# Kernel optimization log

Hardware: AMD Instinct MI355X
Metric: run time of the kernel (lower is better)

Reference implementation:

```python
import jax, jax.numpy as jnp
import numpy as np

F_FRAMES = 128   # number of frames (seq_start_end rows)
P_PEDS = 32      # pedestrians per frame (uniform)
B = F_FRAMES * P_PEDS
E, H, BN, PM, M = 64, 128, 1024, 512, 1024
PRED_LEN = 12


def setup_inputs() -> dict:
    key = jax.random.key(0)
    ks = jax.random.split(key, 20)
    n = lambda k, s, sc=0.05: (jax.random.normal(k, s) * sc).astype(jnp.float32)
    starts = jnp.arange(F_FRAMES, dtype=jnp.int32) * P_PEDS
    seq_start_end = jnp.stack([starts, starts + P_PEDS], axis=1)
    return {
        "h0": n(ks[0], (1, B, H), 1.0),
        "c0": n(ks[1], (1, B, H), 1.0),
        "obs_final_pos": n(ks[2], (B, 2), 1.0),
        "obs_final_pos_rel": n(ks[3], (B, 2), 1.0),
        "W_emb": n(ks[4], (2, E)), "b_emb": jnp.zeros((E,), jnp.float32),
        "W_ih": n(ks[5], (4 * H, E)), "W_hh": n(ks[6], (4 * H, H)),
        "b_ih": jnp.zeros((4 * H,), jnp.float32), "b_hh": jnp.zeros((4 * H,), jnp.float32),
        "W_pos": n(ks[7], (H, 2)), "b_pos": jnp.zeros((2,), jnp.float32),
        "W_pe": n(ks[8], (2, E)), "b_pe": jnp.zeros((E,), jnp.float32),
        "W_p1": n(ks[9], (E + H, PM)), "b_p1": jnp.zeros((PM,), jnp.float32),
        "W_p2": n(ks[10], (PM, BN)), "b_p2": jnp.zeros((BN,), jnp.float32),
        "W_m1": n(ks[11], (H + BN, M)), "b_m1": jnp.zeros((M,), jnp.float32),
        "W_m2": n(ks[12], (M, H)), "b_m2": jnp.zeros((H,), jnp.float32),
        "seq_start_end": seq_start_end,
    }


def reference(h0, c0, obs_final_pos, obs_final_pos_rel,
              W_emb, b_emb, W_ih, W_hh, b_ih, b_hh, W_pos, b_pos,
              W_pe, b_pe, W_p1, b_p1, W_p2, b_p2, W_m1, b_m1, W_m2, b_m2,
              seq_start_end):
    Bn = h0.shape[1]
    F = seq_start_end.shape[0]
    P = Bn // F  # uniform frame size
    h, c = h0[0], c0[0]
    x0 = obs_final_pos_rel @ W_emb + b_emb  # decoder input embedding

    def step(carry, _):
        x, h, c, last_pos = carry
        # LSTM cell (PyTorch gate order i,f,g,o)
        gates = x @ W_ih.T + h @ W_hh.T + b_ih + b_hh  # (B, 4H)
        i, f, g, o = jnp.split(gates, 4, axis=-1)
        i, f, o = jax.nn.sigmoid(i), jax.nn.sigmoid(f), jax.nn.sigmoid(o)
        c_new = f * c + i * jnp.tanh(g)
        h_new = o * jnp.tanh(c_new)
        rel_pos = h_new @ W_pos + b_pos
        curr_pos = rel_pos + last_pos
        # PoolNet: per-frame pairwise rel-pos embed + MLP + max over neighbours j
        pos = curr_pos.reshape(F, P, 2)
        hf = h_new.reshape(F, P, H)
        rel = pos[:, None, :, :] - pos[:, :, None, :]  # rel[f,i,j] = pos_j - pos_i
        e = rel @ W_pe + b_pe  # (F,P,P,E)
        feat = jnp.concatenate(
            [e, jnp.broadcast_to(hf[:, None], (F, P, P, H))], axis=-1)  # h of j
        z = jax.nn.relu(feat @ W_p1 + b_p1)
        z = jax.nn.relu(z @ W_p2 + b_p2)  # (F,P,P,BN)
        pool_h = z.max(axis=2).reshape(Bn, BN)
        # hidden refresh MLP
        mi = jnp.concatenate([h_new, pool_h], axis=-1)
        nh = jax.nn.relu(mi @ W_m1 + b_m1)
        nh = jax.nn.relu(nh @ W_m2 + b_m2)
        x_new = rel_pos @ W_emb + b_emb
        return (x_new, nh, c_new, curr_pos), (curr_pos, rel_pos)

    _, (pred_seq, pred_seq_rel) = jax.lax.scan(
        jax.checkpoint(step), (x0, h, c, obs_final_pos), None, length=PRED_LEN)
    return pred_seq, pred_seq_rel
```

## Files before the change

kernel.cpp:

```cpp
#include <hip/hip_runtime.h>

#define NB 4096
#define HD 128
#define ED 64
#define NF 128
#define NP 32
#define TSTEPS 12

typedef __attribute__((ext_vector_type(8))) short short8;
typedef __attribute__((ext_vector_type(8))) __bf16 bf16x8;
typedef __attribute__((ext_vector_type(8))) _Float16 f16x8;
typedef __attribute__((ext_vector_type(4))) float f32x4;
typedef __attribute__((ext_vector_type(16))) float f32x16;

#define MFMA16(a, b, c)  __builtin_amdgcn_mfma_f32_16x16x32_bf16((a), (b), (c), 0, 0, 0)
#define MFMA32H(a, b, c) __builtin_amdgcn_mfma_f32_32x32x16_f16((a), (b), (c), 0, 0, 0)

__device__ __forceinline__ unsigned short f2bf(float f) {
  unsigned int x = __float_as_uint(f);
  x += 0x7fffu + ((x >> 16) & 1u);
  return (unsigned short)(x >> 16);
}

__device__ __forceinline__ float sigm(float x) { return 1.0f / (1.0f + expf(-x)); }

__device__ __forceinline__ f16x8 relu8(f16x8 x) {
  return __builtin_elementwise_max(x, (f16x8)(_Float16)0);
}


__global__ __launch_bounds__(256) void k_transpose_bf(const float* __restrict__ W,
                                                      unsigned short* __restrict__ Wt,
                                                      int K, int N) {
  __shared__ float t[32][33];
  int nb = blockIdx.x * 32, kb = blockIdx.y * 32;
  int tx = threadIdx.x & 31, ty = threadIdx.x >> 5;
  #pragma unroll
  for (int r = 0; r < 32; r += 8)
    t[ty + r][tx] = W[(size_t)(kb + ty + r) * N + nb + tx];
  __syncthreads();
  #pragma unroll
  for (int r = 0; r < 32; r += 8)
    Wt[(size_t)(nb + ty + r) * K + kb + tx] = f2bf(t[tx][ty + r]);
}

__global__ __launch_bounds__(256) void k_pack_bfrag32(const float* __restrict__ Wp2,
                                                      _Float16* __restrict__ Bf) {
  int U = blockIdx.x * 256 + threadIdx.x;
  int l = U & 63, cb = (U >> 6) & 31, ks = U >> 11;
  int col = cb * 32 + (l & 31);
  int k0 = ks * 16 + (l >> 5) * 8;
  f16x8 r;
  #pragma unroll
  for (int e = 0; e < 8; ++e) r[e] = (_Float16)Wp2[(size_t)(k0 + e) * 1024 + col];
  *(f16x8*)(Bf + (size_t)U * 8) = r;
}

__global__ __launch_bounds__(256) void k_pack_lstm_w(const float* __restrict__ Wih,
                                                     const float* __restrict__ Whh,
                                                     float* __restrict__ WihT,
                                                     float* __restrict__ WhhT) {
  int idx = blockIdx.x * 256 + threadIdx.x;
  if (idx < 64 * 512) { int k = idx >> 9, n = idx & 511; WihT[idx] = Wih[n * 64 + k]; }
  if (idx < 128 * 512) { int k = idx >> 9, n = idx & 511; WhhT[idx] = Whh[n * 128 + k]; }
}

__global__ __launch_bounds__(256) void k_pack_wpp(const float* __restrict__ Wpe,
                                                  const float* __restrict__ bpe,
                                                  const float* __restrict__ Wp1,
                                                  const float* __restrict__ bp1,
                                                  float* __restrict__ Wpp,
                                                  float* __restrict__ cvec) {
  int n = blockIdx.x * 256 + threadIdx.x;
  if (n >= 512) return;
  float s0 = 0.f, s1 = 0.f, sc = 0.f;
  for (int k = 0; k < 64; ++k) {
    float w = Wp1[k * 512 + n];
    s0 += Wpe[k] * w;
    s1 += Wpe[64 + k] * w;
    sc += bpe[k] * w;
  }
  Wpp[n * 2] = s0; Wpp[n * 2 + 1] = s1; cvec[n] = sc + bp1[n];
}

__global__ __launch_bounds__(256) void k_x0(const float* __restrict__ ofr,
                                            const float* __restrict__ Wemb,
                                            const float* __restrict__ bemb,
                                            float* __restrict__ x) {
  int idx = blockIdx.x * 256 + threadIdx.x;
  if (idx >= NB * ED) return;
  int row = idx >> 6, e = idx & 63;
  x[idx] = bemb[e] + ofr[row * 2] * Wemb[e] + ofr[row * 2 + 1] * Wemb[64 + e];
}


__global__ __launch_bounds__(256) void k12_lstm_uv(
    const float* __restrict__ x, const float* __restrict__ hin, const float* __restrict__ cin,
    const float* __restrict__ WihT, const float* __restrict__ WhhT,
    const float* __restrict__ bih, const float* __restrict__ bhh,
    const float* __restrict__ Wpos, const float* __restrict__ bpos,
    const float* __restrict__ Wemb, const float* __restrict__ bemb,
    const float* __restrict__ lastpos,
    const float* __restrict__ Wp1, const float* __restrict__ Wpp,
    const float* __restrict__ cvec,
    float* __restrict__ cout, unsigned short* __restrict__ mi,
    float* __restrict__ posout, float* __restrict__ xout,
    float* __restrict__ outc, float* __restrict__ outr,
    _Float16* __restrict__ u16, _Float16* __restrict__ v16) {
  __shared__ float xh[8][192];
  __shared__ float hnl[8][128];
  __shared__ float rp[8][2];
  __shared__ float cp[8][2];
  int tid = threadIdx.x;
  int r0 = blockIdx.x * 8;
  for (int idx = tid; idx < 8 * 192; idx += 256) {
    int r = idx / 192, k = idx % 192;
    xh[r][k] = (k < 64) ? x[(r0 + r) * 64 + k] : hin[(r0 + r) * 128 + (k - 64)];
  }
  __syncthreads();
  int j = tid & 127, rg = tid >> 7;
  float acc0[4], acc1[4], acc2[4], acc3[4];
  {
    float b0 = bih[j] + bhh[j];
    float b1 = bih[128 + j] + bhh[128 + j];
    float b2 = bih[256 + j] + bhh[256 + j];
    float b3 = bih[384 + j] + bhh[384 + j];
    #pragma unroll
    for (int r = 0; r < 4; ++r) { acc0[r] = b0; acc1[r] = b1; acc2[r] = b2; acc3[r] = b3; }
  }
  for (int k = 0; k < 64; ++k) {
    float w0 = WihT[k * 512 + j], w1 = WihT[k * 512 + 128 + j],
          w2 = WihT[k * 512 + 256 + j], w3 = WihT[k * 512 + 384 + j];
    #pragma unroll
    for (int r = 0; r < 4; ++r) {
      float xv = xh[rg * 4 + r][k];
      acc0[r] += w0 * xv; acc1[r] += w1 * xv; acc2[r] += w2 * xv; acc3[r] += w3 * xv;
    }
  }
  for (int k = 0; k < 128; ++k) {
    float w0 = WhhT[k * 512 + j], w1 = WhhT[k * 512 + 128 + j],
          w2 = WhhT[k * 512 + 256 + j], w3 = WhhT[k * 512 + 384 + j];
    #pragma unroll
    for (int r = 0; r < 4; ++r) {
      float hv = xh[rg * 4 + r][64 + k];
      acc0[r] += w0 * hv; acc1[r] += w1 * hv; acc2[r] += w2 * hv; acc3[r] += w3 * hv;
    }
  }
  #pragma unroll
  for (int r = 0; r < 4; ++r) {
    int row = r0 + rg * 4 + r;
    float ig = sigm(acc0[r]), fg = sigm(acc1[r]), gg = tanhf(acc2[r]), og = sigm(acc3[r]);
    float cn = fg * cin[row * 128 + j] + ig * gg;
    float hv = og * tanhf(cn);
    cout[row * 128 + j] = cn;
    mi[(size_t)row * 1152 + j] = f2bf(hv);
    hnl[rg * 4 + r][j] = hv;
  }
  __syncthreads();
  {
    int r = tid >> 5;
    int d = (tid >> 4) & 1;
    int l = tid & 15;
    float s = 0.f;
    #pragma unroll
    for (int k = l; k < 128; k += 16) s += hnl[r][k] * Wpos[k * 2 + d];
    s += __shfl_xor(s, 1);
    s += __shfl_xor(s, 2);
    s += __shfl_xor(s, 4);
    s += __shfl_xor(s, 8);
    if (l == 0) {
      int row = r0 + r;
      float rel = s + bpos[d];
      float cur = rel + lastpos[row * 2 + d];
      rp[r][d] = rel;
      cp[r][d] = cur;
      posout[row * 2 + d] = cur;
      outc[row * 2 + d] = cur;
      outr[row * 2 + d] = rel;
    }
  }
  __syncthreads();
  for (int idx = tid; idx < 8 * 64; idx += 256) {
    int r = idx >> 6, e = idx & 63;
    xout[(r0 + r) * 64 + e] = bemb[e] + rp[r][0] * Wemb[e] + rp[r][1] * Wemb[64 + e];
  }
  int n = tid, n2 = tid + 256;
  float aA[8], aB[8];
  #pragma unroll
  for (int r = 0; r < 8; ++r) { aA[r] = 0.f; aB[r] = 0.f; }
  for (int k = 0; k < 128; ++k) {
    float wA = Wp1[(64 + k) * 512 + n], wB = Wp1[(64 + k) * 512 + n2];
    #pragma unroll
    for (int r = 0; r < 8; ++r) { aA[r] += wA * hnl[r][k]; aB[r] += wB * hnl[r][k]; }
  }
  float wp0A = Wpp[n * 2], wp1A = Wpp[n * 2 + 1], cA = cvec[n];
  float wp0B = Wpp[n2 * 2], wp1B = Wpp[n2 * 2 + 1], cB = cvec[n2];
  #pragma unroll
  for (int r = 0; r < 8; ++r) {
    int row = r0 + r;
    float t0 = cp[r][0] * wp0A + cp[r][1] * wp1A;
    v16[(size_t)row * 512 + n] = (_Float16)t0;
    u16[(size_t)row * 512 + n] = (_Float16)(t0 + aA[r] + cA);
    float t1 = cp[r][0] * wp0B + cp[r][1] * wp1B;
    v16[(size_t)row * 512 + n2] = (_Float16)t1;
    u16[(size_t)row * 512 + n2] = (_Float16)(t1 + aB[r] + cB);
  }
}

__global__ __launch_bounds__(256, 2) void k3_pool(
    const _Float16* __restrict__ u16, const _Float16* __restrict__ v16,
    const _Float16* __restrict__ Bf, const float* __restrict__ bp2,
    unsigned short* __restrict__ mi) {
  __shared__ _Float16 u_lds[32 * 512];
  __shared__ _Float16 v_lds[8 * 512];
  int f = blockIdx.x, ig = blockIdx.y, ng = blockIdx.z;
  int tid = threadIdx.x, wid = tid >> 6, lane = tid & 63;
  int r32 = lane & 31, hi = lane >> 5;
  int ip = wid >> 1, nh = wid & 1;

  const f16x8* Bfu = (const f16x8*)Bf;
  int cb0 = ng * 4 + nh * 2;

  f16x8 Bb[8][2];
  #pragma unroll
  for (int s = 0; s < 7; ++s) {
    Bb[s][0] = Bfu[(size_t)((s * 32 + cb0 + 0) * 64 + lane)];
    Bb[s][1] = Bfu[(size_t)((s * 32 + cb0 + 1) * 64 + lane)];
  }

  #pragma unroll
  for (int t = 0; t < 8; ++t) {
    int unit = tid + t * 256;
    int row = unit >> 6, seg = unit & 63;
    f16x8 val = *(const f16x8*)(u16 + (size_t)(f * 32 + row) * 512 + seg * 8);
    int byte = (row << 10) + (seg << 4);
    byte ^= (row & 7) << 4;
    *(f16x8*)((char*)u_lds + byte) = val;
  }
  #pragma unroll
  for (int t = 0; t < 2; ++t) {
    int unit = tid + t * 256;
    int row = unit >> 6, seg = unit & 63;
    *(f16x8*)(v_lds + (row << 9) + seg * 8) =
        *(const f16x8*)(v16 + (size_t)(f * 32 + ig * 8 + row) * 512 + seg * 8);
  }
  __syncthreads();

  f32x16 acc[4][2];
  #pragma unroll
  for (int a = 0; a < 4; ++a)
    #pragma unroll
    for (int n = 0; n < 2; ++n)
      #pragma unroll
      for (int r = 0; r < 16; ++r) acc[a][n][r] = 0.f;

  int ubase = (r32 << 10) + (hi << 4);
  int usw = (r32 & 7) << 4;
  const _Float16* vp = v_lds + ((ip * 4) << 9) + hi * 8;

#define K3STEP(KS)                                                               \
  {                                                                              \
    if ((KS) + 7 < 32) {                                                         \
      Bb[((KS) + 7) & 7][0] = Bfu[(size_t)((((KS) + 7) * 32 + cb0 + 0) * 64 + lane)]; \
      Bb[((KS) + 7) & 7][1] = Bfu[(size_t)((((KS) + 7) * 32 + cb0 + 1) * 64 + lane)]; \
    }                                                                            \
    f16x8 uf = *(const f16x8*)((const char*)u_lds + ((ubase + (KS) * 32) ^ usw));\
    f16x8 a0 = relu8(uf - *(const f16x8*)(vp + (KS) * 16));                      \
    f16x8 a1 = relu8(uf - *(const f16x8*)(vp + 512 + (KS) * 16));                \
    f16x8 a2 = relu8(uf - *(const f16x8*)(vp + 1024 + (KS) * 16));               \
    f16x8 a3 = relu8(uf - *(const f16x8*)(vp + 1536 + (KS) * 16));               \
    __builtin_amdgcn_s_setprio(1);                                               \
    acc[0][0] = MFMA32H(a0, Bb[(KS) & 7][0], acc[0][0]);                         \
    acc[1][0] = MFMA32H(a1, Bb[(KS) & 7][0], acc[1][0]);                         \
    acc[2][0] = MFMA32H(a2, Bb[(KS) & 7][0], acc[2][0]);                         \
    acc[3][0] = MFMA32H(a3, Bb[(KS) & 7][0], acc[3][0]);                         \
    acc[0][1] = MFMA32H(a0, Bb[(KS) & 7][1], acc[0][1]);                         \
    acc[1][1] = MFMA32H(a1, Bb[(KS) & 7][1], acc[1][1]);                         \
    acc[2][1] = MFMA32H(a2, Bb[(KS) & 7][1], acc[2][1]);                         \
    acc[3][1] = MFMA32H(a3, Bb[(KS) & 7][1], acc[3][1]);                         \
    __builtin_amdgcn_s_setprio(0);                                               \
  }

  #pragma unroll
  for (int kk = 0; kk < 32; kk += 8) {
    K3STEP(kk + 0) K3STEP(kk + 1) K3STEP(kk + 2) K3STEP(kk + 3)
    K3STEP(kk + 4) K3STEP(kk + 5) K3STEP(kk + 6) K3STEP(kk + 7)
  }
#undef K3STEP

  #pragma unroll
  for (int ii = 0; ii < 4; ++ii) {
    int rowg = f * 32 + ig * 8 + ip * 4 + ii;
    #pragma unroll
    for (int nt = 0; nt < 2; ++nt) {
      float m = acc[ii][nt][0];
      #pragma unroll
      for (int r = 1; r < 16; ++r) m = fmaxf(m, acc[ii][nt][r]);
      m = fmaxf(m, __shfl_xor(m, 32));
      if (hi == 0) {
        int col = (cb0 + nt) * 32 + r32;
        float val = fmaxf(m + bp2[col], 0.f);
        mi[(size_t)rowg * 1152 + 128 + col] = f2bf(val);
      }
    }
  }
}

__global__ __launch_bounds__(512) void k4_mlp1(
    const unsigned short* __restrict__ mi, const unsigned short* __restrict__ Wt,
    const float* __restrict__ bm1, unsigned short* __restrict__ nh1) {
  int bid = blockIdx.x;
  int mb = bid & 63, nb = bid >> 6;
  int tid = threadIdx.x, wid = tid >> 6, lane = tid & 63;
  int row0 = mb * 64 + (wid >> 2) * 32;
  int nc0 = nb * 256 + (wid & 3) * 64;
  int c = lane & 15, q = lane >> 4;
  const unsigned short* a0p = mi + (size_t)(row0 + c) * 1152;
  const unsigned short* a1p = a0p + 16 * 1152;
  const unsigned short* bb = Wt + (size_t)(nc0 + c) * 1152;
  f32x4 acc[2][4];
  #pragma unroll
  for (int a = 0; a < 2; ++a)
    #pragma unroll
    for (int b = 0; b < 4; ++b) acc[a][b] = (f32x4){0.f, 0.f, 0.f, 0.f};
  for (int ks = 0; ks < 36; ++ks) {
    int k0 = ks * 32 + q * 8;
    bf16x8 a0 = *(const bf16x8*)(a0p + k0);
    bf16x8 a1 = *(const bf16x8*)(a1p + k0);
    #pragma unroll
    for (int nt = 0; nt < 4; ++nt) {
      bf16x8 bf = *(const bf16x8*)(bb + (size_t)nt * 16 * 1152 + k0);
      acc[0][nt] = MFMA16(a0, bf, acc[0][nt]);
      acc[1][nt] = MFMA16(a1, bf, acc[1][nt]);
    }
  }
  #pragma unroll
  for (int mt = 0; mt < 2; ++mt)
    #pragma unroll
    for (int nt = 0; nt < 4; ++nt)
      #pragma unroll
      for (int r = 0; r < 4; ++r) {
        int row = row0 + mt * 16 + q * 4 + r;
        int col = nc0 + nt * 16 + c;
        float val = fmaxf(acc[mt][nt][r] + bm1[col], 0.f);
        nh1[(size_t)row * 1024 + col] = f2bf(val);
      }
}

__global__ __launch_bounds__(128) void k5_mlp2(
    const unsigned short* __restrict__ nh1, const unsigned short* __restrict__ Wt,
    const float* __restrict__ bm2, float* __restrict__ hout) {
  int bid = blockIdx.x;
  int tid = threadIdx.x, wid = tid >> 6, lane = tid & 63;
  int row0 = bid * 16;
  int nc0 = wid * 64;
  int c = lane & 15, q = lane >> 4;
  const unsigned short* ap = nh1 + (size_t)(row0 + c) * 1024;
  const unsigned short* bb = Wt + (size_t)(nc0 + c) * 1024;
  f32x4 acc[4];
  #pragma unroll
  for (int b = 0; b < 4; ++b) acc[b] = (f32x4){0.f, 0.f, 0.f, 0.f};
  for (int ks = 0; ks < 32; ++ks) {
    int k0 = ks * 32 + q * 8;
    bf16x8 a = *(const bf16x8*)(ap + k0);
    #pragma unroll
    for (int nt = 0; nt < 4; ++nt) {
      bf16x8 bf = *(const bf16x8*)(bb + (size_t)nt * 16 * 1024 + k0);
      acc[nt] = MFMA16(a, bf, acc[nt]);
    }
  }
  #pragma unroll
  for (int nt = 0; nt < 4; ++nt)
    #pragma unroll
    for (int r = 0; r < 4; ++r) {
      int row = row0 + q * 4 + r;
      int col = nc0 + nt * 16 + c;
      hout[(size_t)row * 128 + col] = fmaxf(acc[nt][r] + bm2[col], 0.f);
    }
}


extern "C" void kernel_launch(void* const* d_in, const int* in_sizes, int n_in,
                              void* d_out, int out_size, void* d_ws, size_t ws_size,
                              hipStream_t stream) {
  const float* h0   = (const float*)d_in[0];
  const float* c0   = (const float*)d_in[1];
  const float* ofp  = (const float*)d_in[2];
  const float* ofr  = (const float*)d_in[3];
  const float* Wemb = (const float*)d_in[4];
  const float* bemb = (const float*)d_in[5];
  const float* Wih  = (const float*)d_in[6];
  const float* Whh  = (const float*)d_in[7];
  const float* bih  = (const float*)d_in[8];
  const float* bhh  = (const float*)d_in[9];
  const float* Wpos = (const float*)d_in[10];
  const float* bpos = (const float*)d_in[11];
  const float* Wpe  = (const float*)d_in[12];
  const float* bpe  = (const float*)d_in[13];
  const float* Wp1  = (const float*)d_in[14];
  const float* bp1  = (const float*)d_in[15];
  const float* Wp2  = (const float*)d_in[16];
  const float* bp2  = (const float*)d_in[17];
  const float* Wm1  = (const float*)d_in[18];
  const float* bm1  = (const float*)d_in[19];
  const float* Wm2  = (const float*)d_in[20];
  const float* bm2  = (const float*)d_in[21];

  char* ws = (char*)d_ws;
  size_t off = 0;
  auto alloc = [&](size_t bytes) {
    char* p = ws + off;
    off += (bytes + 255) & ~(size_t)255;
    return p;
  };
  float* h    = (float*)alloc((size_t)NB * HD * 4);
  float* cst  = (float*)alloc((size_t)NB * HD * 4);
  float* xbuf = (float*)alloc((size_t)NB * ED * 4);
  float* pos  = (float*)alloc((size_t)NB * 2 * 4);
  _Float16* u16 = (_Float16*)alloc((size_t)NB * 512 * 2);
  _Float16* v16 = (_Float16*)alloc((size_t)NB * 512 * 2);
  unsigned short* mi   = (unsigned short*)alloc((size_t)NB * 1152 * 2);
  unsigned short* nh1  = (unsigned short*)alloc((size_t)NB * 1024 * 2);
  float* WihT = (float*)alloc(64 * 512 * 4);
  float* WhhT = (float*)alloc(128 * 512 * 4);
  float* Wpp  = (float*)alloc(512 * 2 * 4);
  float* cvec = (float*)alloc(512 * 4);
  _Float16* Bf  = (_Float16*)alloc((size_t)1024 * 512 * 2);
  unsigned short* Wm1t = (unsigned short*)alloc((size_t)1024 * 1152 * 2);
  unsigned short* Wm2t = (unsigned short*)alloc((size_t)128 * 1024 * 2);

  float* outc = (float*)d_out;
  float* outr = outc + (size_t)TSTEPS * NB * 2;

  k_pack_lstm_w<<<256, 256, 0, stream>>>(Wih, Whh, WihT, WhhT);
  k_pack_wpp<<<2, 256, 0, stream>>>(Wpe, bpe, Wp1, bp1, Wpp, cvec);
  k_pack_bfrag32<<<256, 256, 0, stream>>>(Wp2, Bf);
  k_transpose_bf<<<dim3(1024 / 32, 1152 / 32), 256, 0, stream>>>(Wm1, Wm1t, 1152, 1024);
  k_transpose_bf<<<dim3(128 / 32, 1024 / 32), 256, 0, stream>>>(Wm2, Wm2t, 1024, 128);
  k_x0<<<NB * ED / 256, 256, 0, stream>>>(ofr, Wemb, bemb, xbuf);

  for (int t = 0; t < TSTEPS; ++t) {
    const float* hin = (t == 0) ? h0 : h;
    const float* cin = (t == 0) ? c0 : cst;
    const float* lp  = (t == 0) ? ofp : pos;
    k12_lstm_uv<<<NB / 8, 256, 0, stream>>>(xbuf, hin, cin, WihT, WhhT, bih, bhh,
                                            Wpos, bpos, Wemb, bemb, lp, Wp1, Wpp, cvec,
                                            cst, mi, pos, xbuf,
                                            outc + (size_t)t * NB * 2,
                                            outr + (size_t)t * NB * 2, u16, v16);
    k3_pool<<<dim3(128, 4, 8), 256, 0, stream>>>(u16, v16, Bf, bp2, mi);
    k4_mlp1<<<256, 512, 0, stream>>>(mi, Wm1t, bm1, nh1);
    k5_mlp2<<<256, 128, 0, stream>>>(nh1, Wm2t, bm2, h);
  }
}
```

Measured before the change: 2.883 ms.

## Split pool kernel work across 8 waves with smaller per-wave accumulator tiles

The pool kernel now runs with 512 threads per block instead of 256. Each wave handles 2 pedestrian rows instead of 4, which halves its accumulator registers, and the B-fragment prefetch depth drops from 7 to 3. The aim is more resident waves per CU to hide LDS and global latency. In exchange, the Wp2 fragments are loaded by twice as many waves, and the shallower prefetch may expose more of the global load latency.

```diff
diff --git a/kernel.cpp b/kernel.cpp
--- a/kernel.cpp
+++ b/kernel.cpp
@@ -207,7 +207,7 @@
   }
 }
 
-__global__ __launch_bounds__(256, 2) void k3_pool(
+__global__ __launch_bounds__(512, 4) void k3_pool(
     const _Float16* __restrict__ u16, const _Float16* __restrict__ v16,
     const _Float16* __restrict__ Bf, const float* __restrict__ bp2,
     unsigned short* __restrict__ mi) {
@@ -221,34 +221,32 @@
   const f16x8* Bfu = (const f16x8*)Bf;
   int cb0 = ng * 4 + nh * 2;
 
-  f16x8 Bb[8][2];
-  #pragma unroll
-  for (int s = 0; s < 7; ++s) {
+  f16x8 Bb[4][2];
+  #pragma unroll
+  for (int s = 0; s < 3; ++s) {
     Bb[s][0] = Bfu[(size_t)((s * 32 + cb0 + 0) * 64 + lane)];
     Bb[s][1] = Bfu[(size_t)((s * 32 + cb0 + 1) * 64 + lane)];
   }
 
   #pragma unroll
-  for (int t = 0; t < 8; ++t) {
-    int unit = tid + t * 256;
+  for (int t = 0; t < 4; ++t) {
+    int unit = tid + t * 512;
     int row = unit >> 6, seg = unit & 63;
     f16x8 val = *(const f16x8*)(u16 + (size_t)(f * 32 + row) * 512 + seg * 8);
     int byte = (row << 10) + (seg << 4);
     byte ^= (row & 7) << 4;
     *(f16x8*)((char*)u_lds + byte) = val;
   }
-  #pragma unroll
-  for (int t = 0; t < 2; ++t) {
-    int unit = tid + t * 256;
-    int row = unit >> 6, seg = unit & 63;
+  {
+    int row = tid >> 6, seg = tid & 63;
     *(f16x8*)(v_lds + (row << 9) + seg * 8) =
         *(const f16x8*)(v16 + (size_t)(f * 32 + ig * 8 + row) * 512 + seg * 8);
   }
   __syncthreads();
 
-  f32x16 acc[4][2];
-  #pragma unroll
-  for (int a = 0; a < 4; ++a)
+  f32x16 acc[2][2];
+  #pragma unroll
+  for (int a = 0; a < 2; ++a)
     #pragma unroll
     for (int n = 0; n < 2; ++n)
       #pragma unroll
@@ -256,41 +254,28 @@
 
   int ubase = (r32 << 10) + (hi << 4);
   int usw = (r32 & 7) << 4;
-  const _Float16* vp = v_lds + ((ip * 4) << 9) + hi * 8;
-
-#define K3STEP(KS)                                                               \
-  {                                                                              \
-    if ((KS) + 7 < 32) {                                                         \
-      Bb[((KS) + 7) & 7][0] = Bfu[(size_t)((((KS) + 7) * 32 + cb0 + 0) * 64 + lane)]; \
-      Bb[((KS) + 7) & 7][1] = Bfu[(size_t)((((KS) + 7) * 32 + cb0 + 1) * 64 + lane)]; \
-    }                                                                            \
-    f16x8 uf = *(const f16x8*)((const char*)u_lds + ((ubase + (KS) * 32) ^ usw));\
-    f16x8 a0 = relu8(uf - *(const f16x8*)(vp + (KS) * 16));                      \
-    f16x8 a1 = relu8(uf - *(const f16x8*)(vp + 512 + (KS) * 16));                \
-    f16x8 a2 = relu8(uf - *(const f16x8*)(vp + 1024 + (KS) * 16));               \
-    f16x8 a3 = relu8(uf - *(const f16x8*)(vp + 1536 + (KS) * 16));               \
-    __builtin_amdgcn_s_setprio(1);                                               \
-    acc[0][0] = MFMA32H(a0, Bb[(KS) & 7][0], acc[0][0]);                         \
-    acc[1][0] = MFMA32H(a1, Bb[(KS) & 7][0], acc[1][0]);                         \
-    acc[2][0] = MFMA32H(a2, Bb[(KS) & 7][0], acc[2][0]);                         \
-    acc[3][0] = MFMA32H(a3, Bb[(KS) & 7][0], acc[3][0]);                         \
-    acc[0][1] = MFMA32H(a0, Bb[(KS) & 7][1], acc[0][1]);                         \
-    acc[1][1] = MFMA32H(a1, Bb[(KS) & 7][1], acc[1][1]);                         \
-    acc[2][1] = MFMA32H(a2, Bb[(KS) & 7][1], acc[2][1]);                         \
-    acc[3][1] = MFMA32H(a3, Bb[(KS) & 7][1], acc[3][1]);                         \
-    __builtin_amdgcn_s_setprio(0);                                               \
-  }
-
-  #pragma unroll
-  for (int kk = 0; kk < 32; kk += 8) {
-    K3STEP(kk + 0) K3STEP(kk + 1) K3STEP(kk + 2) K3STEP(kk + 3)
-    K3STEP(kk + 4) K3STEP(kk + 5) K3STEP(kk + 6) K3STEP(kk + 7)
-  }
-#undef K3STEP
-
-  #pragma unroll
-  for (int ii = 0; ii < 4; ++ii) {
-    int rowg = f * 32 + ig * 8 + ip * 4 + ii;
+  const _Float16* vp = v_lds + ((ip * 2) << 9) + hi * 8;
+
+  #pragma unroll
+  for (int ks = 0; ks < 32; ++ks) {
+    if (ks + 3 < 32) {
+      Bb[(ks + 3) & 3][0] = Bfu[(size_t)(((ks + 3) * 32 + cb0 + 0) * 64 + lane)];
+      Bb[(ks + 3) & 3][1] = Bfu[(size_t)(((ks + 3) * 32 + cb0 + 1) * 64 + lane)];
+    }
+    f16x8 uf = *(const f16x8*)((const char*)u_lds + ((ubase + ks * 32) ^ usw));
+    f16x8 a0 = relu8(uf - *(const f16x8*)(vp + ks * 16));
+    f16x8 a1 = relu8(uf - *(const f16x8*)(vp + 512 + ks * 16));
+    __builtin_amdgcn_s_setprio(1);
+    acc[0][0] = MFMA32H(a0, Bb[ks & 3][0], acc[0][0]);
+    acc[1][0] = MFMA32H(a1, Bb[ks & 3][0], acc[1][0]);
+    acc[0][1] = MFMA32H(a0, Bb[ks & 3][1], acc[0][1]);
+    acc[1][1] = MFMA32H(a1, Bb[ks & 3][1], acc[1][1]);
+    __builtin_amdgcn_s_setprio(0);
+  }
+
+  #pragma unroll
+  for (int ii = 0; ii < 2; ++ii) {
+    int rowg = f * 32 + ig * 8 + ip * 2 + ii;
     #pragma unroll
     for (int nt = 0; nt < 2; ++nt) {
       float m = acc[ii][nt][0];
@@ -448,7 +433,7 @@
                                             cst, mi, pos, xbuf,
                                             outc + (size_t)t * NB * 2,
                                             outr + (size_t)t * NB * 2, u16, v16);
-    k3_pool<<<dim3(128, 4, 8), 256, 0, stream>>>(u16, v16, Bf, bp2, mi);
+    k3_pool<<<dim3(128, 4, 8), 512, 0, stream>>>(u16, v16, Bf, bp2, mi);
     k4_mlp1<<<256, 512, 0, stream>>>(mi, Wm1t, bm1, nh1);
     k5_mlp2<<<256, 128, 0, stream>>>(nh1, Wm2t, bm2, h);
   }
```

After: 2.990 ms. +3.7%, slower.
